# Optimization experiments

Measured on AMD Instinct MI355X. Metric: run time of the kernel, lower is better.

Reference implementation:

```python
import jax, jax.numpy as jnp
import numpy as np

V, H, O = 50257, 512, 4
B, T = 64, 512


def setup_inputs() -> dict:
    key = jax.random.key(0)
    ks = jax.random.split(key, 8)
    s = 1.0 / np.sqrt(H)
    return {
        "input_ids": jax.random.randint(ks[0], (B, T), 0, V),
        "labels": jax.random.randint(ks[1], (B,), 0, O),
        "emb": jax.random.normal(ks[2], (V, H), dtype=jnp.float32) * s,
        "W_in": jax.random.normal(ks[3], (H, H), dtype=jnp.float32) * s,   # linear_input.weight [out,in], no bias
        "W_h": jax.random.normal(ks[4], (H, H), dtype=jnp.float32) * s,    # linear_hidden.weight
        "b_h": jax.random.normal(ks[5], (H,), dtype=jnp.float32) * s,      # linear_hidden.bias
        "W_out": jax.random.normal(ks[6], (O, H), dtype=jnp.float32) * s,  # linear_output.weight
        "b_out": jax.random.normal(ks[7], (O,), dtype=jnp.float32) * s,
    }


def reference(input_ids, labels, emb, W_in, W_h, b_h, W_out, b_out):
    # Embed all tokens up front: [B, T, H] -> scan over time [T, B, H]
    x = emb[input_ids]
    xs = jnp.swapaxes(x, 0, 1)
    h0 = jnp.zeros((input_ids.shape[0], W_h.shape[0]), dtype=emb.dtype)

    def step(h, x_t):
        # Elman cell: relu(x W_in^T + h W_h^T + b_h)
        h_new = jax.nn.relu(x_t @ W_in.T + h @ W_h.T + b_h)
        return h_new, None

    h_T, _ = jax.lax.scan(step, h0, xs)
    # NOTE: original applies Softmax BEFORE CrossEntropyLoss (faithful bug reproduction)
    logits = jax.nn.softmax(h_T @ W_out.T + b_out, axis=1)
    logp = jax.nn.log_softmax(logits, axis=1)
    loss = -jnp.take_along_axis(logp, labels[:, None], axis=1).mean()
    return loss, logits
```

## Files before the change

### kernel.cpp

```cpp
#include <hip/hip_runtime.h>


typedef _Float16 f16;
typedef _Float16 half2_t __attribute__((ext_vector_type(2)));
typedef _Float16 half8_t __attribute__((ext_vector_type(8)));
typedef float f32x4 __attribute__((ext_vector_type(4)));
typedef unsigned int u32x4 __attribute__((ext_vector_type(4)));

#define HDIM 512
#define BATCH 64
#define TSTEPS 512
#define OUTC 4

__device__ __forceinline__ float dot2f(unsigned int h, unsigned int w, float acc) {
#if __has_builtin(__builtin_amdgcn_fdot2)
  return __builtin_amdgcn_fdot2(__builtin_bit_cast(half2_t, h),
                                __builtin_bit_cast(half2_t, w), acc, false);
#else
  half2_t a = __builtin_bit_cast(half2_t, h);
  half2_t b = __builtin_bit_cast(half2_t, w);
  return acc + (float)a.x * (float)b.x + (float)a.y * (float)b.y;
#endif
}

__global__ void convert_w(const float* __restrict__ Win, const float* __restrict__ Wh,
                          f16* __restrict__ wif, f16* __restrict__ whf) {
  int i = blockIdx.x * 256 + threadIdx.x;
  if (i < HDIM * HDIM) {
    wif[i] = (f16)Win[i];
    whf[i] = (f16)Wh[i];
  }
}

__global__ __launch_bounds__(256) void embed_f16(const int* __restrict__ ids,
                                                 const float* __restrict__ emb,
                                                 f16* __restrict__ xh) {
  int gid = blockIdx.x * 256 + threadIdx.x;
  int r = gid >> 7;
  int lane = gid & 127;
  int id = ids[(r & 63) * TSTEPS + (r >> 6)];
  float4 a = *(const float4*)(emb + id * HDIM + lane * 4);
  half2_t lo, hi;
  lo.x = (f16)a.x; lo.y = (f16)a.y;
  hi.x = (f16)a.z; hi.y = (f16)a.w;
  half2_t* dst = (half2_t*)(xh + r * HDIM + lane * 4);
  dst[0] = lo;
  dst[1] = hi;
}

__global__ __launch_bounds__(256) void gemm_pre(const f16* __restrict__ xh,
                                                const f16* __restrict__ wif,
                                                const float* __restrict__ bh,
                                                f16* __restrict__ preh) {
  __shared__ __align__(16) f16 Al[64][40];
  __shared__ __align__(16) f16 Bl[64][40];

  const int tid = threadIdx.x;
  const int rb = blockIdx.x;
  const int nb = blockIdx.y;
  const int w = tid >> 6;
  const int l = tid & 63;

  f32x4 acc[4] = {};

  const int srow = tid >> 2;
  const int quad = tid & 3;

  for (int k0 = 0; k0 < HDIM; k0 += 32) {
    *(u32x4*)&Al[srow][quad * 8] =
        *(const u32x4*)(xh + (rb * 64 + srow) * HDIM + k0 + quad * 8);
    *(u32x4*)&Bl[srow][quad * 8] =
        *(const u32x4*)(wif + (nb * 64 + srow) * HDIM + k0 + quad * 8);
    __syncthreads();

    half8_t af = *(const half8_t*)&Al[w * 16 + (l & 15)][(l >> 4) * 8];
#pragma unroll
    for (int nt = 0; nt < 4; ++nt) {
      half8_t bf = *(const half8_t*)&Bl[nt * 16 + (l & 15)][(l >> 4) * 8];
      acc[nt] = __builtin_amdgcn_mfma_f32_16x16x32_f16(af, bf, acc[nt], 0, 0, 0);
    }
    __syncthreads();
  }

#pragma unroll
  for (int nt = 0; nt < 4; ++nt) {
#pragma unroll
    for (int i = 0; i < 4; ++i) {
      int r = rb * 64 + w * 16 + (l >> 4) * 4 + i;
      int c = nb * 64 + nt * 16 + (l & 15);
      preh[r * HDIM + c] = (f16)(acc[nt][i] + bh[c]);
    }
  }
}

__global__ __launch_bounds__(512, 2) void rnn_steps(const f16* __restrict__ preh,
                                                    const f16* __restrict__ whf,
                                                    float* __restrict__ hT) {
  __shared__ __align__(16) u32x4 wlds[HDIM * 16];
  __shared__ __align__(16) unsigned int hb[2][HDIM / 2];

  const int j = threadIdx.x;
  const int b = blockIdx.x;

  for (int q = 0; q < 16; ++q) {
    int idx = q * 512 + j;
    int row = idx >> 4, c = idx & 15;
    u32x4 v = *(const u32x4*)(whf + row * HDIM + 384 + c * 8);
    wlds[row * 16 + (c ^ (row & 15))] = v;
  }

  unsigned int wr[192];
  {
    const u32x4* wrow = (const u32x4*)(whf + j * HDIM);
#pragma unroll
    for (int c = 0; c < 48; ++c) {
      u32x4 v = wrow[c];
      wr[4 * c + 0] = v[0];
      wr[4 * c + 1] = v[1];
      wr[4 * c + 2] = v[2];
      wr[4 * c + 3] = v[3];
    }
  }
#pragma unroll
  for (int c = 0; c < 192; c += 4)
    asm volatile("" : "+v"(wr[c]), "+v"(wr[c + 1]), "+v"(wr[c + 2]), "+v"(wr[c + 3]));

  if (j < HDIM / 2) hb[0][j] = 0u;
  __syncthreads();

  float pre_cur = (float)preh[b * HDIM + j];
  for (int t = 0; t < TSTEPS; ++t) {
    float pre_next = 0.f;
    if (t < TSTEPS - 1) pre_next = (float)preh[((t + 1) * BATCH + b) * HDIM + j];

    const u32x4* hp = (const u32x4*)hb[t & 1];
    float acc = pre_cur;
#pragma unroll
    for (int c = 0; c < 48; ++c) {
      u32x4 h4 = hp[c];
      acc = dot2f(h4[0], wr[4 * c + 0], acc);
      acc = dot2f(h4[1], wr[4 * c + 1], acc);
      acc = dot2f(h4[2], wr[4 * c + 2], acc);
      acc = dot2f(h4[3], wr[4 * c + 3], acc);
    }
    const u32x4* wl = &wlds[j * 16];
    const int sw = j & 15;
#pragma unroll
    for (int c = 0; c < 16; ++c) {
      u32x4 h4 = hp[48 + c];
      u32x4 w4 = wl[c ^ sw];
      acc = dot2f(h4[0], w4[0], acc);
      acc = dot2f(h4[1], w4[1], acc);
      acc = dot2f(h4[2], w4[2], acc);
      acc = dot2f(h4[3], w4[3], acc);
    }
    acc = fmaxf(acc, 0.f);
    ((f16*)hb[(t + 1) & 1])[j] = (f16)acc;
    if (t == TSTEPS - 1) hT[b * HDIM + j] = acc;
    pre_cur = pre_next;
    __syncthreads();
  }
}

__global__ void tail_kernel(const float* __restrict__ hT, const float* __restrict__ Wout,
                            const float* __restrict__ bout, const int* __restrict__ labels,
                            float* __restrict__ out) {
  __shared__ float lred[BATCH];
  const int b = threadIdx.x;
  const float4* hr = (const float4*)(hT + b * HDIM);
  const float4* w0 = (const float4*)(Wout + 0 * HDIM);
  const float4* w1 = (const float4*)(Wout + 1 * HDIM);
  const float4* w2 = (const float4*)(Wout + 2 * HDIM);
  const float4* w3 = (const float4*)(Wout + 3 * HDIM);
  float z0 = bout[0], z1 = bout[1], z2 = bout[2], z3 = bout[3];
#pragma unroll 4
  for (int k = 0; k < HDIM / 4; ++k) {
    float4 h = hr[k];
    float4 a = w0[k], c = w1[k], d = w2[k], e = w3[k];
    z0 += h.x * a.x + h.y * a.y + h.z * a.z + h.w * a.w;
    z1 += h.x * c.x + h.y * c.y + h.z * c.z + h.w * c.w;
    z2 += h.x * d.x + h.y * d.y + h.z * d.z + h.w * d.w;
    z3 += h.x * e.x + h.y * e.y + h.z * e.z + h.w * e.w;
  }
  float m = fmaxf(fmaxf(z0, z1), fmaxf(z2, z3));
  float e0 = __expf(z0 - m), e1 = __expf(z1 - m), e2 = __expf(z2 - m), e3 = __expf(z3 - m);
  float se = e0 + e1 + e2 + e3;
  float p0 = e0 / se, p1 = e1 / se, p2 = e2 / se, p3 = e3 / se;
  float m2 = fmaxf(fmaxf(p0, p1), fmaxf(p2, p3));
  float s2 = __expf(p0 - m2) + __expf(p1 - m2) + __expf(p2 - m2) + __expf(p3 - m2);
  float lse = m2 + __logf(s2);
  int lab = labels[b];
  float pl = (lab == 0) ? p0 : (lab == 1) ? p1 : (lab == 2) ? p2 : p3;
  lred[b] = pl - lse;
  out[1 + b * 4 + 0] = p0;
  out[1 + b * 4 + 1] = p1;
  out[1 + b * 4 + 2] = p2;
  out[1 + b * 4 + 3] = p3;
  __syncthreads();
  if (b == 0) {
    float s = 0.f;
#pragma unroll
    for (int i = 0; i < BATCH; ++i) s += lred[i];
    out[0] = -s / (float)BATCH;
  }
}

extern "C" void kernel_launch(void* const* d_in, const int* in_sizes, int n_in,
                              void* d_out, int out_size, void* d_ws, size_t ws_size,
                              hipStream_t stream) {
  const int* ids = (const int*)d_in[0];
  const int* labels = (const int*)d_in[1];
  const float* emb = (const float*)d_in[2];
  const float* Win = (const float*)d_in[3];
  const float* Wh = (const float*)d_in[4];
  const float* bh = (const float*)d_in[5];
  const float* Wout = (const float*)d_in[6];
  const float* bout = (const float*)d_in[7];
  float* out = (float*)d_out;

  char* ws = (char*)d_ws;
  f16* whf = (f16*)ws;
  f16* wif = (f16*)(ws + (512 << 10));
  f16* preh = (f16*)(ws + (1 << 20));
  f16* xh = (f16*)(ws + (1 << 20) + (32 << 20));
  float* hT = (float*)(ws + (1 << 20) + (64 << 20));

  convert_w<<<dim3(1024), dim3(256), 0, stream>>>(Win, Wh, wif, whf);
  embed_f16<<<dim3((BATCH * TSTEPS * 128) / 256), dim3(256), 0, stream>>>(ids, emb, xh);
  gemm_pre<<<dim3(512, 8), dim3(256), 0, stream>>>(xh, wif, bh, preh);
  rnn_steps<<<dim3(64), dim3(512), 0, stream>>>(preh, whf, hT);
  tail_kernel<<<dim3(1), dim3(64), 0, stream>>>(hT, Wout, bout, labels, out);
}
```

Measured before the change: 1.187 ms.

## Halve RNN block threads, two outputs per thread with weights in AGPRs

The recurrent kernel now runs 256 threads per batch row instead of 512. Each thread computes two hidden outputs, so every h vector loaded from LDS serves two weight rows. One row's register-resident weights are pinned to accumulation registers (AGPRs) and the other's to VGPRs, which fits twice the weight state per thread. This cuts LDS reads of h and the number of waves that meet at each step barrier. The costs are a longer serial dependency chain per thread, fewer waves to hide latency, and likely extra AGPR-to-VGPR moves before each dot product.

```diff
diff --git a/kernel.cpp b/kernel.cpp
--- a/kernel.cpp
+++ b/kernel.cpp
@@ -62,7 +62,6 @@
   const int l = tid & 63;
 
   f32x4 acc[4] = {};
-
   const int srow = tid >> 2;
   const int quad = tid & 3;
 
@@ -93,71 +92,103 @@
   }
 }
 
-__global__ __launch_bounds__(512, 2) void rnn_steps(const f16* __restrict__ preh,
+__global__ __launch_bounds__(256, 1) void rnn_steps(const f16* __restrict__ preh,
                                                     const f16* __restrict__ whf,
                                                     float* __restrict__ hT) {
   __shared__ __align__(16) u32x4 wlds[HDIM * 16];
   __shared__ __align__(16) unsigned int hb[2][HDIM / 2];
 
-  const int j = threadIdx.x;
+  const int l = threadIdx.x;
   const int b = blockIdx.x;
 
-  for (int q = 0; q < 16; ++q) {
-    int idx = q * 512 + j;
+  for (int q = 0; q < 32; ++q) {
+    int idx = q * 256 + l;
     int row = idx >> 4, c = idx & 15;
     u32x4 v = *(const u32x4*)(whf + row * HDIM + 384 + c * 8);
     wlds[row * 16 + (c ^ (row & 15))] = v;
   }
 
-  unsigned int wr[192];
+  unsigned int wa[192], wv[192];
   {
-    const u32x4* wrow = (const u32x4*)(whf + j * HDIM);
+    const u32x4* ra = (const u32x4*)(whf + l * HDIM);
 #pragma unroll
     for (int c = 0; c < 48; ++c) {
-      u32x4 v = wrow[c];
-      wr[4 * c + 0] = v[0];
-      wr[4 * c + 1] = v[1];
-      wr[4 * c + 2] = v[2];
-      wr[4 * c + 3] = v[3];
+      u32x4 v = ra[c];
+      unsigned int x0 = v[0], x1 = v[1], x2 = v[2], x3 = v[3];
+      asm volatile("" : "+a"(x0), "+a"(x1), "+a"(x2), "+a"(x3));
+      wa[4 * c + 0] = x0; wa[4 * c + 1] = x1;
+      wa[4 * c + 2] = x2; wa[4 * c + 3] = x3;
+    }
+    const u32x4* rv = (const u32x4*)(whf + (l + 256) * HDIM);
+#pragma unroll
+    for (int c = 0; c < 48; ++c) {
+      u32x4 v = rv[c];
+      wv[4 * c + 0] = v[0]; wv[4 * c + 1] = v[1];
+      wv[4 * c + 2] = v[2]; wv[4 * c + 3] = v[3];
     }
   }
 #pragma unroll
   for (int c = 0; c < 192; c += 4)
-    asm volatile("" : "+v"(wr[c]), "+v"(wr[c + 1]), "+v"(wr[c + 2]), "+v"(wr[c + 3]));
-
-  if (j < HDIM / 2) hb[0][j] = 0u;
+    asm volatile("" : "+v"(wv[c]), "+v"(wv[c + 1]), "+v"(wv[c + 2]), "+v"(wv[c + 3]));
+#pragma unroll
+  for (int c = 0; c < 192; c += 4)
+    asm volatile("" : "+a"(wa[c]), "+a"(wa[c + 1]), "+a"(wa[c + 2]), "+a"(wa[c + 3]));
+
+  hb[0][l] = 0u;
   __syncthreads();
 
-  float pre_cur = (float)preh[b * HDIM + j];
+  float pre0 = (float)preh[b * HDIM + l];
+  float pre1 = (float)preh[b * HDIM + l + 256];
+  const u32x4* wl0 = &wlds[l * 16];
+  const u32x4* wl1 = &wlds[(l + 256) * 16];
+  const int sw = l & 15;
+
   for (int t = 0; t < TSTEPS; ++t) {
-    float pre_next = 0.f;
-    if (t < TSTEPS - 1) pre_next = (float)preh[((t + 1) * BATCH + b) * HDIM + j];
+    float pre0n = 0.f, pre1n = 0.f;
+    if (t < TSTEPS - 1) {
+      pre0n = (float)preh[((t + 1) * BATCH + b) * HDIM + l];
+      pre1n = (float)preh[((t + 1) * BATCH + b) * HDIM + l + 256];
+    }
 
     const u32x4* hp = (const u32x4*)hb[t & 1];
-    float acc = pre_cur;
+    float a0 = pre0, a1 = pre1;
 #pragma unroll
     for (int c = 0; c < 48; ++c) {
       u32x4 h4 = hp[c];
-      acc = dot2f(h4[0], wr[4 * c + 0], acc);
-      acc = dot2f(h4[1], wr[4 * c + 1], acc);
-      acc = dot2f(h4[2], wr[4 * c + 2], acc);
-      acc = dot2f(h4[3], wr[4 * c + 3], acc);
-    }
-    const u32x4* wl = &wlds[j * 16];
-    const int sw = j & 15;
+      a0 = dot2f(h4[0], wa[4 * c + 0], a0);
+      a0 = dot2f(h4[1], wa[4 * c + 1], a0);
+      a0 = dot2f(h4[2], wa[4 * c + 2], a0);
+      a0 = dot2f(h4[3], wa[4 * c + 3], a0);
+      a1 = dot2f(h4[0], wv[4 * c + 0], a1);
+      a1 = dot2f(h4[1], wv[4 * c + 1], a1);
+      a1 = dot2f(h4[2], wv[4 * c + 2], a1);
+      a1 = dot2f(h4[3], wv[4 * c + 3], a1);
+    }
 #pragma unroll
     for (int c = 0; c < 16; ++c) {
       u32x4 h4 = hp[48 + c];
-      u32x4 w4 = wl[c ^ sw];
-      acc = dot2f(h4[0], w4[0], acc);
-      acc = dot2f(h4[1], w4[1], acc);
-      acc = dot2f(h4[2], w4[2], acc);
-      acc = dot2f(h4[3], w4[3], acc);
-    }
-    acc = fmaxf(acc, 0.f);
-    ((f16*)hb[(t + 1) & 1])[j] = (f16)acc;
-    if (t == TSTEPS - 1) hT[b * HDIM + j] = acc;
-    pre_cur = pre_next;
+      u32x4 w0 = wl0[c ^ sw];
+      u32x4 w1 = wl1[c ^ sw];
+      a0 = dot2f(h4[0], w0[0], a0);
+      a0 = dot2f(h4[1], w0[1], a0);
+      a0 = dot2f(h4[2], w0[2], a0);
+      a0 = dot2f(h4[3], w0[3], a0);
+      a1 = dot2f(h4[0], w1[0], a1);
+      a1 = dot2f(h4[1], w1[1], a1);
+      a1 = dot2f(h4[2], w1[2], a1);
+      a1 = dot2f(h4[3], w1[3], a1);
+    }
+    a0 = fmaxf(a0, 0.f);
+    a1 = fmaxf(a1, 0.f);
+    f16* nb = (f16*)hb[(t + 1) & 1];
+    nb[l] = (f16)a0;
+    nb[l + 256] = (f16)a1;
+    if (t == TSTEPS - 1) {
+      hT[b * HDIM + l] = a0;
+      hT[b * HDIM + l + 256] = a1;
+    }
+    pre0 = pre0n;
+    pre1 = pre1n;
     __syncthreads();
   }
 }
@@ -228,6 +259,6 @@
   convert_w<<<dim3(1024), dim3(256), 0, stream>>>(Win, Wh, wif, whf);
   embed_f16<<<dim3((BATCH * TSTEPS * 128) / 256), dim3(256), 0, stream>>>(ids, emb, xh);
   gemm_pre<<<dim3(512, 8), dim3(256), 0, stream>>>(xh, wif, bh, preh);
-  rnn_steps<<<dim3(64), dim3(512), 0, stream>>>(preh, whf, hT);
+  rnn_steps<<<dim3(64), dim3(256), 0, stream>>>(preh, whf, hT);
   tail_kernel<<<dim3(1), dim3(64), 0, stream>>>(hT, Wout, bout, labels, out);
 }
```

Result: slower. 3.355 ms (+182.6%).
